# Kernel tuning notes

Hardware: AMD Instinct MI355X
Metric: run time of the kernel (lower is better)

Reference implementation:

```python
import jax, jax.numpy as jnp
import numpy as np

EPSILON = 1e-8
TAU = 0.1

def setup_inputs() -> dict:
    key = jax.random.key(0)
    x = jax.random.normal(key, (8192, 256), dtype=jnp.float32)
    return {"x": x}

def reference(x):
    # L2-normalize rows (torch F.normalize: x / max(||x||, 1e-12))
    norm = jnp.maximum(jnp.linalg.norm(x, axis=1, keepdims=True), 1e-12)
    xn = x / norm
    n = xn.shape[0]
    # pairwise cosine similarity via GEMM (equivalent to broadcast sum in source)
    cos = (xn @ xn.T) / TAU                      # [N, N]
    exp_cos = jnp.exp(cos)
    # zero out diagonal (self-similarity)
    exp_cos = exp_cos * (1.0 - jnp.eye(n, dtype=exp_cos.dtype))
    loss = jnp.log(exp_cos.sum(axis=1) / (n - 1) + EPSILON)
    return jnp.mean(loss)
```

## Files before the change

kernel.cpp:

```cpp
#include <hip/hip_runtime.h>
#include <hip/hip_bf16.h>
#include <math.h>

#define TAU_INV_LOG2E 14.4269504088896340736f
#define EPS 1e-8f

typedef __attribute__((ext_vector_type(8))) short bf16x8;
typedef __attribute__((ext_vector_type(4))) float f32x4;

static __device__ __forceinline__ unsigned short f2bf(float f) {
    unsigned int u = __float_as_uint(f);
    unsigned int r = (u + 0x7fffu + ((u >> 16) & 1u)) >> 16;
    return (unsigned short)r;
}

static __device__ __forceinline__ void glds16(const void* g, void* l) {
    __builtin_amdgcn_global_load_lds(
        (const __attribute__((address_space(1))) unsigned int*)g,
        (__attribute__((address_space(3))) unsigned int*)l,
        16, 0, 0);
}

__global__ __launch_bounds__(256) void normalize_kernel(
    const float* __restrict__ x, unsigned short* __restrict__ xn,
    float* __restrict__ out, int N) {
    const int wave = threadIdx.x >> 6;
    const int lane = threadIdx.x & 63;
    const int row  = blockIdx.x * 4 + wave;
    if (row >= N) return;

    if (blockIdx.x == 0 && threadIdx.x == 0) out[0] = 0.0f;

    const float4 v = ((const float4*)(x + (size_t)row * 256))[lane];
    float s = v.x * v.x + v.y * v.y + v.z * v.z + v.w * v.w;
    s += __shfl_xor(s, 1);
    s += __shfl_xor(s, 2);
    s += __shfl_xor(s, 4);
    s += __shfl_xor(s, 8);
    s += __shfl_xor(s, 16);
    s += __shfl_xor(s, 32);
    const float norm = fmaxf(sqrtf(s), 1e-12f);
    const float rinv = 1.0f / norm;

    ushort4 o;
    o.x = f2bf(v.x * rinv);
    o.y = f2bf(v.y * rinv);
    o.z = f2bf(v.z * rinv);
    o.w = f2bf(v.w * rinv);
    ((ushort4*)(xn + (size_t)row * 256))[lane] = o;
}

__global__ __launch_bounds__(256, 3) void gemm_exp_rowsum_kernel(
    const unsigned short* __restrict__ xn, float* __restrict__ prow, int N) {
    const int D = 256;
    __shared__ unsigned short As[2][128 * 32];
    __shared__ unsigned short Bs[2][128 * 32];

    const int tid   = threadIdx.x;
    const int wave  = tid >> 6;
    const int lane  = tid & 63;
    const int waveM = wave >> 1;
    const int waveN = wave & 1;
    const int quad  = lane >> 4;
    const int l16   = lane & 15;

    const int B = N >> 7;
    const int t = blockIdx.x;
    int bi = (int)((2.0 * B + 1.0 -
                    sqrt((2.0 * B + 1.0) * (2.0 * B + 1.0) - 8.0 * (double)t)) * 0.5);
    while (bi > 0 && t < bi * B - (bi * (bi - 1)) / 2) --bi;
    while (t >= (bi + 1) * B - ((bi + 1) * bi) / 2) ++bi;
    const int bj = bi + (t - (bi * B - (bi * (bi - 1)) / 2));
    const bool diag = (bi == bj);

    const int iBase = bi * 128;
    const int jBase = bj * 128;

    f32x4 acc[4][4];
    #pragma unroll
    for (int mt = 0; mt < 4; ++mt)
        #pragma unroll
        for (int nt = 0; nt < 4; ++nt)
            acc[mt][nt] = (f32x4){0.f, 0.f, 0.f, 0.f};

    const int lrow4 = lane >> 2;
    const int csrc  = (lane & 3) ^ ((lane >> 3) & 3);

    auto stage = [&](int buf, int k0) {
        #pragma unroll
        for (int it = 0; it < 2; ++it) {
            const int w = wave * 2 + it;
            const int r = w * 16 + lrow4;
            glds16(xn + (size_t)(iBase + r) * D + k0 + csrc * 8,
                   &As[buf][w * 512]);
            if (!diag)
                glds16(xn + (size_t)(jBase + r) * D + k0 + csrc * 8,
                       &Bs[buf][w * 512]);
        }
    };

    const int swz  = (quad ^ ((l16 >> 1) & 3)) * 8;
    const int offA = (waveM * 64 + l16) * 32 + swz;
    const int offB = (waveN * 64 + l16) * 32 + swz;
    const unsigned short* Bbase = diag ? &As[0][0] : &Bs[0][0];

    stage(0, 0);
    __syncthreads();

    #pragma unroll
    for (int kt = 0; kt < 8; ++kt) {
        const int cb = kt & 1;
        if (kt < 7) stage(cb ^ 1, (kt + 1) * 32);

        const unsigned short* Ap = &As[cb][0];
        const unsigned short* Bp = Bbase + cb * (128 * 32);
        bf16x8 a[4], b[4];
        #pragma unroll
        for (int tt = 0; tt < 4; ++tt) {
            a[tt] = *(const bf16x8*)(Ap + offA + tt * 512);
            b[tt] = *(const bf16x8*)(Bp + offB + tt * 512);
        }
        #pragma unroll
        for (int mt = 0; mt < 4; ++mt)
            #pragma unroll
            for (int nt = 0; nt < 4; ++nt)
                acc[mt][nt] = __builtin_amdgcn_mfma_f32_16x16x32_bf16(
                    a[mt], b[nt], acc[mt][nt], 0, 0, 0);

        if (kt < 7) __syncthreads();
    }

    float rsum[4][4];
    float csum[4] = {0.f, 0.f, 0.f, 0.f};
    #pragma unroll
    for (int mt = 0; mt < 4; ++mt)
        #pragma unroll
        for (int r = 0; r < 4; ++r) rsum[mt][r] = 0.f;

    #pragma unroll
    for (int mt = 0; mt < 4; ++mt) {
        const int gi0 = iBase + waveM * 64 + mt * 16 + quad * 4;
        #pragma unroll
        for (int nt = 0; nt < 4; ++nt) {
            const int gj = jBase + waveN * 64 + nt * 16 + l16;
            #pragma unroll
            for (int r = 0; r < 4; ++r) {
                float e = __builtin_amdgcn_exp2f(acc[mt][nt][r] * TAU_INV_LOG2E);
                if (gi0 + r == gj) e = 0.0f;
                rsum[mt][r] += e;
                csum[nt] += e;
            }
        }
    }
    {
        float* slot = prow + (size_t)(2 * bj + waveN) * N;
        #pragma unroll
        for (int mt = 0; mt < 4; ++mt) {
            const int gi0 = iBase + waveM * 64 + mt * 16 + quad * 4;
            #pragma unroll
            for (int r = 0; r < 4; ++r) {
                float s = rsum[mt][r];
                s += __shfl_xor(s, 1);
                s += __shfl_xor(s, 2);
                s += __shfl_xor(s, 4);
                s += __shfl_xor(s, 8);
                if (l16 == 0) slot[gi0 + r] = s;
            }
        }
    }
    if (!diag) {
        float* slot = prow + (size_t)(2 * bi + waveM) * N;
        #pragma unroll
        for (int nt = 0; nt < 4; ++nt) {
            float s = csum[nt];
            s += __shfl_xor(s, 16);
            s += __shfl_xor(s, 32);
            if (quad == 0)
                slot[jBase + waveN * 64 + nt * 16 + l16] = s;
        }
    }
}

__global__ __launch_bounds__(256) void finalize_kernel(
    const float* __restrict__ prow, float* __restrict__ out, int N) {
    __shared__ float red[4];
    const int i = blockIdx.x * 256 + threadIdx.x;
    const float inv = 1.0f / (float)(N - 1);
    float s = 0.f;
    #pragma unroll 16
    for (int p = 0; p < 128; ++p) s += prow[(size_t)p * N + i];
    float acc = logf(fmaf(s, inv, EPS));
    acc += __shfl_xor(acc, 1);
    acc += __shfl_xor(acc, 2);
    acc += __shfl_xor(acc, 4);
    acc += __shfl_xor(acc, 8);
    acc += __shfl_xor(acc, 16);
    acc += __shfl_xor(acc, 32);
    const int wave = threadIdx.x >> 6;
    const int lane = threadIdx.x & 63;
    if (lane == 0) red[wave] = acc;
    __syncthreads();
    if (threadIdx.x == 0) {
        float total = red[0] + red[1] + red[2] + red[3];
        atomicAdd(out, total / (float)N);
    }
}

extern "C" void kernel_launch(void* const* d_in, const int* in_sizes, int n_in,
                              void* d_out, int out_size, void* d_ws, size_t ws_size,
                              hipStream_t stream) {
    const float* x = (const float*)d_in[0];
    const int D = 256;
    const int N = in_sizes[0] / D;

    unsigned short* xn = (unsigned short*)d_ws;
    float* prow = (float*)((char*)d_ws + (size_t)N * D * sizeof(unsigned short));
    float* out = (float*)d_out;

    normalize_kernel<<<(N + 3) / 4, 256, 0, stream>>>(x, xn, out, N);

    const int B = N / 128;
    const int T = B * (B + 1) / 2;
    gemm_exp_rowsum_kernel<<<T, 256, 0, stream>>>(xn, prow, N);

    finalize_kernel<<<N / 256, 256, 0, stream>>>(prow, out, N);
}
```

Baseline: 95.84 us.

## Process strips of four column tiles per block with A fragments held in registers

Each block now owns one row tile and walks up to four upper-triangle column tiles. The A operand fragments stay in registers across all of them, and B fragments are read straight from global memory, so the LDS staging and barriers are gone. Row partial sums are accumulated across the strip, which cuts the number of partial-sum slots, and the finalize kernel is reworked to read variable counts of row and column partials. The cost is higher register pressure (occupancy hint drops to 2), fewer blocks, and uncoalesced 16-byte global B loads with no LDS reuse between waves.

```diff
diff --git a/kernel.cpp b/kernel.cpp
--- a/kernel.cpp
+++ b/kernel.cpp
@@ -12,13 +12,6 @@
     unsigned int u = __float_as_uint(f);
     unsigned int r = (u + 0x7fffu + ((u >> 16) & 1u)) >> 16;
     return (unsigned short)r;
-}
-
-static __device__ __forceinline__ void glds16(const void* g, void* l) {
-    __builtin_amdgcn_global_load_lds(
-        (const __attribute__((address_space(1))) unsigned int*)g,
-        (__attribute__((address_space(3))) unsigned int*)l,
-        16, 0, 0);
 }
 
 __global__ __launch_bounds__(256) void normalize_kernel(
@@ -50,12 +43,10 @@
     ((ushort4*)(xn + (size_t)row * 256))[lane] = o;
 }
 
-__global__ __launch_bounds__(256, 3) void gemm_exp_rowsum_kernel(
-    const unsigned short* __restrict__ xn, float* __restrict__ prow, int N) {
+__global__ __launch_bounds__(256, 2) void gemm_strip_kernel(
+    const unsigned short* __restrict__ xn, float* __restrict__ prowR,
+    float* __restrict__ prowC, float* __restrict__ out, int N) {
     const int D = 256;
-    __shared__ unsigned short As[2][128 * 32];
-    __shared__ unsigned short Bs[2][128 * 32];
-
     const int tid   = threadIdx.x;
     const int wave  = tid >> 6;
     const int lane  = tid & 63;
@@ -65,95 +56,87 @@
     const int l16   = lane & 15;
 
     const int B = N >> 7;
-    const int t = blockIdx.x;
-    int bi = (int)((2.0 * B + 1.0 -
-                    sqrt((2.0 * B + 1.0) * (2.0 * B + 1.0) - 8.0 * (double)t)) * 0.5);
-    while (bi > 0 && t < bi * B - (bi * (bi - 1)) / 2) --bi;
-    while (t >= (bi + 1) * B - ((bi + 1) * bi) / 2) ++bi;
-    const int bj = bi + (t - (bi * B - (bi * (bi - 1)) / 2));
-    const bool diag = (bi == bj);
-
+    int rem = blockIdx.x, bi = 0;
+    while (rem >= ((B - bi + 3) >> 2)) { rem -= (B - bi + 3) >> 2; ++bi; }
+    const int sid   = rem;
+    const int bj0   = bi + (sid << 2);
+    const int bjEnd = min(bj0 + 3, B - 1);
     const int iBase = bi * 128;
-    const int jBase = bj * 128;
-
-    f32x4 acc[4][4];
+
+    bf16x8 afr[8][4];
+    {
+        const unsigned short* aBase =
+            xn + (size_t)(iBase + waveM * 64 + l16) * D + quad * 8;
+        #pragma unroll
+        for (int kc = 0; kc < 8; ++kc)
+            #pragma unroll
+            for (int tt = 0; tt < 4; ++tt)
+                afr[kc][tt] = *(const bf16x8*)(aBase + (size_t)tt * 16 * D + kc * 32);
+    }
+
+    float rsum[4][4];
     #pragma unroll
     for (int mt = 0; mt < 4; ++mt)
         #pragma unroll
-        for (int nt = 0; nt < 4; ++nt)
-            acc[mt][nt] = (f32x4){0.f, 0.f, 0.f, 0.f};
-
-    const int lrow4 = lane >> 2;
-    const int csrc  = (lane & 3) ^ ((lane >> 3) & 3);
-
-    auto stage = [&](int buf, int k0) {
-        #pragma unroll
-        for (int it = 0; it < 2; ++it) {
-            const int w = wave * 2 + it;
-            const int r = w * 16 + lrow4;
-            glds16(xn + (size_t)(iBase + r) * D + k0 + csrc * 8,
-                   &As[buf][w * 512]);
-            if (!diag)
-                glds16(xn + (size_t)(jBase + r) * D + k0 + csrc * 8,
-                       &Bs[buf][w * 512]);
-        }
-    };
-
-    const int swz  = (quad ^ ((l16 >> 1) & 3)) * 8;
-    const int offA = (waveM * 64 + l16) * 32 + swz;
-    const int offB = (waveN * 64 + l16) * 32 + swz;
-    const unsigned short* Bbase = diag ? &As[0][0] : &Bs[0][0];
-
-    stage(0, 0);
-    __syncthreads();
-
-    #pragma unroll
-    for (int kt = 0; kt < 8; ++kt) {
-        const int cb = kt & 1;
-        if (kt < 7) stage(cb ^ 1, (kt + 1) * 32);
-
-        const unsigned short* Ap = &As[cb][0];
-        const unsigned short* Bp = Bbase + cb * (128 * 32);
-        bf16x8 a[4], b[4];
-        #pragma unroll
-        for (int tt = 0; tt < 4; ++tt) {
-            a[tt] = *(const bf16x8*)(Ap + offA + tt * 512);
-            b[tt] = *(const bf16x8*)(Bp + offB + tt * 512);
-        }
+        for (int r = 0; r < 4; ++r) rsum[mt][r] = 0.f;
+
+    for (int bj = bj0; bj <= bjEnd; ++bj) {
+        const int jBase = bj * 128;
+        const unsigned short* bBase =
+            xn + (size_t)(jBase + waveN * 64 + l16) * D + quad * 8;
+
+        f32x4 acc[4][4];
         #pragma unroll
         for (int mt = 0; mt < 4; ++mt)
             #pragma unroll
             for (int nt = 0; nt < 4; ++nt)
-                acc[mt][nt] = __builtin_amdgcn_mfma_f32_16x16x32_bf16(
-                    a[mt], b[nt], acc[mt][nt], 0, 0, 0);
-
-        if (kt < 7) __syncthreads();
+                acc[mt][nt] = (f32x4){0.f, 0.f, 0.f, 0.f};
+
+        #pragma unroll
+        for (int kc = 0; kc < 8; ++kc) {
+            bf16x8 b[4];
+            #pragma unroll
+            for (int nt = 0; nt < 4; ++nt)
+                b[nt] = *(const bf16x8*)(bBase + (size_t)nt * 16 * D + kc * 32);
+            #pragma unroll
+            for (int mt = 0; mt < 4; ++mt)
+                #pragma unroll
+                for (int nt = 0; nt < 4; ++nt)
+                    acc[mt][nt] = __builtin_amdgcn_mfma_f32_16x16x32_bf16(
+                        afr[kc][mt], b[nt], acc[mt][nt], 0, 0, 0);
+        }
+
+        float csum[4] = {0.f, 0.f, 0.f, 0.f};
+        #pragma unroll
+        for (int mt = 0; mt < 4; ++mt) {
+            const int gi0 = iBase + waveM * 64 + mt * 16 + quad * 4;
+            #pragma unroll
+            for (int nt = 0; nt < 4; ++nt) {
+                const int gj = jBase + waveN * 64 + nt * 16 + l16;
+                #pragma unroll
+                for (int r = 0; r < 4; ++r) {
+                    float e = __builtin_amdgcn_exp2f(acc[mt][nt][r] * TAU_INV_LOG2E);
+                    if (gi0 + r == gj) e = 0.0f;
+                    rsum[mt][r] += e;
+                    csum[nt] += e;
+                }
+            }
+        }
+        if (bj != bi) {
+            float* slot = prowC + (size_t)(2 * bi + waveM) * N;
+            #pragma unroll
+            for (int nt = 0; nt < 4; ++nt) {
+                float s = csum[nt];
+                s += __shfl_xor(s, 16);
+                s += __shfl_xor(s, 32);
+                if (quad == 0)
+                    slot[jBase + waveN * 64 + nt * 16 + l16] = s;
+            }
+        }
     }
 
-    float rsum[4][4];
-    float csum[4] = {0.f, 0.f, 0.f, 0.f};
-    #pragma unroll
-    for (int mt = 0; mt < 4; ++mt)
-        #pragma unroll
-        for (int r = 0; r < 4; ++r) rsum[mt][r] = 0.f;
-
-    #pragma unroll
-    for (int mt = 0; mt < 4; ++mt) {
-        const int gi0 = iBase + waveM * 64 + mt * 16 + quad * 4;
-        #pragma unroll
-        for (int nt = 0; nt < 4; ++nt) {
-            const int gj = jBase + waveN * 64 + nt * 16 + l16;
-            #pragma unroll
-            for (int r = 0; r < 4; ++r) {
-                float e = __builtin_amdgcn_exp2f(acc[mt][nt][r] * TAU_INV_LOG2E);
-                if (gi0 + r == gj) e = 0.0f;
-                rsum[mt][r] += e;
-                csum[nt] += e;
-            }
-        }
-    }
     {
-        float* slot = prow + (size_t)(2 * bj + waveN) * N;
+        float* slot = prowR + (size_t)(2 * sid + waveN) * N;
         #pragma unroll
         for (int mt = 0; mt < 4; ++mt) {
             const int gi0 = iBase + waveM * 64 + mt * 16 + quad * 4;
@@ -168,28 +151,21 @@
             }
         }
     }
-    if (!diag) {
-        float* slot = prow + (size_t)(2 * bi + waveM) * N;
-        #pragma unroll
-        for (int nt = 0; nt < 4; ++nt) {
-            float s = csum[nt];
-            s += __shfl_xor(s, 16);
-            s += __shfl_xor(s, 32);
-            if (quad == 0)
-                slot[jBase + waveN * 64 + nt * 16 + l16] = s;
-        }
-    }
-}
-
-__global__ __launch_bounds__(256) void finalize_kernel(
-    const float* __restrict__ prow, float* __restrict__ out, int N) {
-    __shared__ float red[4];
-    const int i = blockIdx.x * 256 + threadIdx.x;
-    const float inv = 1.0f / (float)(N - 1);
+}
+
+__global__ __launch_bounds__(128) void finalize_kernel(
+    const float* __restrict__ prowR, const float* __restrict__ prowC,
+    float* __restrict__ out, int N) {
+    __shared__ float red[2];
+    const int B = N >> 7;
+    const int a = blockIdx.x;
+    const int i = a * 128 + threadIdx.x;
+    const int nR = 2 * ((B - a + 3) >> 2);
+    const int nC = 2 * a;
     float s = 0.f;
-    #pragma unroll 16
-    for (int p = 0; p < 128; ++p) s += prow[(size_t)p * N + i];
-    float acc = logf(fmaf(s, inv, EPS));
+    for (int p = 0; p < nR; ++p) s += prowR[(size_t)p * N + i];
+    for (int p = 0; p < nC; ++p) s += prowC[(size_t)p * N + i];
+    float acc = logf(fmaf(s, 1.0f / (float)(N - 1), EPS));
     acc += __shfl_xor(acc, 1);
     acc += __shfl_xor(acc, 2);
     acc += __shfl_xor(acc, 4);
@@ -200,10 +176,7 @@
     const int lane = threadIdx.x & 63;
     if (lane == 0) red[wave] = acc;
     __syncthreads();
-    if (threadIdx.x == 0) {
-        float total = red[0] + red[1] + red[2] + red[3];
-        atomicAdd(out, total / (float)N);
-    }
+    if (threadIdx.x == 0) atomicAdd(out, (red[0] + red[1]) / (float)N);
 }
 
 extern "C" void kernel_launch(void* const* d_in, const int* in_sizes, int n_in,
@@ -212,16 +185,18 @@
     const float* x = (const float*)d_in[0];
     const int D = 256;
     const int N = in_sizes[0] / D;
+    const int B = N / 128;
 
     unsigned short* xn = (unsigned short*)d_ws;
-    float* prow = (float*)((char*)d_ws + (size_t)N * D * sizeof(unsigned short));
+    float* prowR = (float*)((char*)d_ws + (size_t)N * D * 2);
+    float* prowC = prowR + (size_t)32 * N;
     float* out = (float*)d_out;
 
     normalize_kernel<<<(N + 3) / 4, 256, 0, stream>>>(x, xn, out, N);
 
-    const int B = N / 128;
-    const int T = B * (B + 1) / 2;
-    gemm_exp_rowsum_kernel<<<T, 256, 0, stream>>>(xn, prow, N);
-
-    finalize_kernel<<<N / 256, 256, 0, stream>>>(prow, out, N);
-}
+    int T = 0;
+    for (int bi = 0; bi < B; ++bi) T += (B - bi + 3) >> 2;
+    gemm_strip_kernel<<<T, 256, 0, stream>>>(xn, prowR, prowC, out, N);
+
+    finalize_kernel<<<B, 128, 0, stream>>>(prowR, prowC, out, N);
+}
```

Measured after the change: 153.2 us. +59.8%, slower.

## Enlarge GEMM tiles to 256x256 with 512 threads and split partial-sum buffers

Applied to the files above, without the earlier changes.

Moves the symmetric GEMM+exp+rowsum kernel from 128x128 tiles with 4 waves to 256x256 tiles with 8 waves, each wave now computing 128x64. K steps grow to 64, and MFMA issue is wrapped in setprio. This raises arithmetic intensity and cuts the number of tile blocks and LDS loads per FLOP. In exchange it uses 128KB of LDS per block, limiting occupancy, and it drops the diagonal-block B-load shortcut. Row and column partials now go to separate buffers, and finalize reads only the slots that were written.

```diff
diff --git a/kernel.cpp b/kernel.cpp
--- a/kernel.cpp
+++ b/kernel.cpp
@@ -50,21 +50,22 @@
     ((ushort4*)(xn + (size_t)row * 256))[lane] = o;
 }
 
-__global__ __launch_bounds__(256, 3) void gemm_exp_rowsum_kernel(
-    const unsigned short* __restrict__ xn, float* __restrict__ prow, int N) {
+__global__ __launch_bounds__(512, 2) void gemm_exp_rowsum_kernel(
+    const unsigned short* __restrict__ xn, float* __restrict__ prowR,
+    float* __restrict__ prowC, int N) {
     const int D = 256;
-    __shared__ unsigned short As[2][128 * 32];
-    __shared__ unsigned short Bs[2][128 * 32];
+    __shared__ unsigned short As[2][256 * 64];
+    __shared__ unsigned short Bs[2][256 * 64];
 
     const int tid   = threadIdx.x;
     const int wave  = tid >> 6;
     const int lane  = tid & 63;
-    const int waveM = wave >> 1;
-    const int waveN = wave & 1;
+    const int waveM = wave >> 2;
+    const int waveN = wave & 3;
     const int quad  = lane >> 4;
     const int l16   = lane & 15;
 
-    const int B = N >> 7;
+    const int B = N >> 8;
     const int t = blockIdx.x;
     int bi = (int)((2.0 * B + 1.0 -
                     sqrt((2.0 * B + 1.0) * (2.0 * B + 1.0) - 8.0 * (double)t)) * 0.5);
@@ -73,73 +74,80 @@
     const int bj = bi + (t - (bi * B - (bi * (bi - 1)) / 2));
     const bool diag = (bi == bj);
 
-    const int iBase = bi * 128;
-    const int jBase = bj * 128;
-
-    f32x4 acc[4][4];
-    #pragma unroll
-    for (int mt = 0; mt < 4; ++mt)
+    const int iBase = bi * 256;
+    const int jBase = bj * 256;
+
+    f32x4 acc[8][4];
+    #pragma unroll
+    for (int mt = 0; mt < 8; ++mt)
         #pragma unroll
         for (int nt = 0; nt < 4; ++nt)
             acc[mt][nt] = (f32x4){0.f, 0.f, 0.f, 0.f};
 
-    const int lrow4 = lane >> 2;
-    const int csrc  = (lane & 3) ^ ((lane >> 3) & 3);
+    const int lrow8 = lane >> 3;
+    const int csrc  = (lane & 7) ^ ((lane >> 3) & 7);
 
     auto stage = [&](int buf, int k0) {
         #pragma unroll
-        for (int it = 0; it < 2; ++it) {
-            const int w = wave * 2 + it;
-            const int r = w * 16 + lrow4;
+        for (int it = 0; it < 4; ++it) {
+            const int r = wave * 32 + it * 8 + lrow8;
             glds16(xn + (size_t)(iBase + r) * D + k0 + csrc * 8,
-                   &As[buf][w * 512]);
-            if (!diag)
-                glds16(xn + (size_t)(jBase + r) * D + k0 + csrc * 8,
-                       &Bs[buf][w * 512]);
+                   &As[buf][(wave * 32 + it * 8) * 64]);
+            glds16(xn + (size_t)(jBase + r) * D + k0 + csrc * 8,
+                   &Bs[buf][(wave * 32 + it * 8) * 64]);
         }
     };
 
-    const int swz  = (quad ^ ((l16 >> 1) & 3)) * 8;
-    const int offA = (waveM * 64 + l16) * 32 + swz;
-    const int offB = (waveN * 64 + l16) * 32 + swz;
-    const unsigned short* Bbase = diag ? &As[0][0] : &Bs[0][0];
+    const int swz0 = ((0 * 4 + quad) ^ (l16 & 7)) * 8;
+    const int swz1 = ((1 * 4 + quad) ^ (l16 & 7)) * 8;
+    const int rowA = waveM * 128 + l16;
+    const int rowB = waveN * 64 + l16;
 
     stage(0, 0);
     __syncthreads();
 
     #pragma unroll
-    for (int kt = 0; kt < 8; ++kt) {
+    for (int kt = 0; kt < 4; ++kt) {
         const int cb = kt & 1;
-        if (kt < 7) stage(cb ^ 1, (kt + 1) * 32);
+        if (kt < 3) stage(cb ^ 1, (kt + 1) * 64);
 
         const unsigned short* Ap = &As[cb][0];
-        const unsigned short* Bp = Bbase + cb * (128 * 32);
-        bf16x8 a[4], b[4];
-        #pragma unroll
-        for (int tt = 0; tt < 4; ++tt) {
-            a[tt] = *(const bf16x8*)(Ap + offA + tt * 512);
-            b[tt] = *(const bf16x8*)(Bp + offB + tt * 512);
-        }
-        #pragma unroll
-        for (int mt = 0; mt < 4; ++mt)
+        const unsigned short* Bp = &Bs[cb][0];
+
+        #pragma unroll
+        for (int ks = 0; ks < 2; ++ks) {
+            const int swz = ks ? swz1 : swz0;
+            bf16x8 a[8], b[4];
+            #pragma unroll
+            for (int mt = 0; mt < 8; ++mt)
+                a[mt] = *(const bf16x8*)(Ap + (rowA + mt * 16) * 64 + swz);
             #pragma unroll
             for (int nt = 0; nt < 4; ++nt)
-                acc[mt][nt] = __builtin_amdgcn_mfma_f32_16x16x32_bf16(
-                    a[mt], b[nt], acc[mt][nt], 0, 0, 0);
-
-        if (kt < 7) __syncthreads();
-    }
-
-    float rsum[4][4];
+                b[nt] = *(const bf16x8*)(Bp + (rowB + nt * 16) * 64 + swz);
+
+            __builtin_amdgcn_s_setprio(1);
+            #pragma unroll
+            for (int mt = 0; mt < 8; ++mt)
+                #pragma unroll
+                for (int nt = 0; nt < 4; ++nt)
+                    acc[mt][nt] = __builtin_amdgcn_mfma_f32_16x16x32_bf16(
+                        a[mt], b[nt], acc[mt][nt], 0, 0, 0);
+            __builtin_amdgcn_s_setprio(0);
+        }
+
+        if (kt < 3) __syncthreads();
+    }
+
+    float rsum[8][4];
     float csum[4] = {0.f, 0.f, 0.f, 0.f};
     #pragma unroll
-    for (int mt = 0; mt < 4; ++mt)
+    for (int mt = 0; mt < 8; ++mt)
         #pragma unroll
         for (int r = 0; r < 4; ++r) rsum[mt][r] = 0.f;
 
     #pragma unroll
-    for (int mt = 0; mt < 4; ++mt) {
-        const int gi0 = iBase + waveM * 64 + mt * 16 + quad * 4;
+    for (int mt = 0; mt < 8; ++mt) {
+        const int gi0 = iBase + waveM * 128 + mt * 16 + quad * 4;
         #pragma unroll
         for (int nt = 0; nt < 4; ++nt) {
             const int gj = jBase + waveN * 64 + nt * 16 + l16;
@@ -153,10 +161,10 @@
         }
     }
     {
-        float* slot = prow + (size_t)(2 * bj + waveN) * N;
-        #pragma unroll
-        for (int mt = 0; mt < 4; ++mt) {
-            const int gi0 = iBase + waveM * 64 + mt * 16 + quad * 4;
+        float* slot = prowR + (size_t)(4 * bj + waveN) * N;
+        #pragma unroll
+        for (int mt = 0; mt < 8; ++mt) {
+            const int gi0 = iBase + waveM * 128 + mt * 16 + quad * 4;
             #pragma unroll
             for (int r = 0; r < 4; ++r) {
                 float s = rsum[mt][r];
@@ -169,7 +177,7 @@
         }
     }
     if (!diag) {
-        float* slot = prow + (size_t)(2 * bi + waveM) * N;
+        float* slot = prowC + (size_t)(2 * bi + waveM) * N;
         #pragma unroll
         for (int nt = 0; nt < 4; ++nt) {
             float s = csum[nt];
@@ -182,14 +190,15 @@
 }
 
 __global__ __launch_bounds__(256) void finalize_kernel(
-    const float* __restrict__ prow, float* __restrict__ out, int N) {
+    const float* __restrict__ prowR, const float* __restrict__ prowC,
+    float* __restrict__ out, int N) {
     __shared__ float red[4];
-    const int i = blockIdx.x * 256 + threadIdx.x;
-    const float inv = 1.0f / (float)(N - 1);
+    const int a = blockIdx.x;
+    const int i = a * 256 + threadIdx.x;
     float s = 0.f;
-    #pragma unroll 16
-    for (int p = 0; p < 128; ++p) s += prow[(size_t)p * N + i];
-    float acc = logf(fmaf(s, inv, EPS));
+    for (int p = 4 * a; p < 128; ++p) s += prowR[(size_t)p * N + i];
+    for (int p = 0; p < 2 * a; ++p)   s += prowC[(size_t)p * N + i];
+    float acc = logf(fmaf(s, 1.0f / (float)(N - 1), EPS));
     acc += __shfl_xor(acc, 1);
     acc += __shfl_xor(acc, 2);
     acc += __shfl_xor(acc, 4);
@@ -200,10 +209,8 @@
     const int lane = threadIdx.x & 63;
     if (lane == 0) red[wave] = acc;
     __syncthreads();
-    if (threadIdx.x == 0) {
-        float total = red[0] + red[1] + red[2] + red[3];
-        atomicAdd(out, total / (float)N);
-    }
+    if (threadIdx.x == 0)
+        atomicAdd(out, (red[0] + red[1] + red[2] + red[3]) / (float)N);
 }
 
 extern "C" void kernel_launch(void* const* d_in, const int* in_sizes, int n_in,
@@ -212,16 +219,17 @@
     const float* x = (const float*)d_in[0];
     const int D = 256;
     const int N = in_sizes[0] / D;
+    const int B = N / 256;
 
     unsigned short* xn = (unsigned short*)d_ws;
-    float* prow = (float*)((char*)d_ws + (size_t)N * D * sizeof(unsigned short));
+    float* prowR = (float*)((char*)d_ws + (size_t)N * D * 2);
+    float* prowC = prowR + (size_t)128 * N;
     float* out = (float*)d_out;
 
     normalize_kernel<<<(N + 3) / 4, 256, 0, stream>>>(x, xn, out, N);
 
-    const int B = N / 128;
     const int T = B * (B + 1) / 2;
-    gemm_exp_rowsum_kernel<<<T, 256, 0, stream>>>(xn, prow, N);
-
-    finalize_kernel<<<N / 256, 256, 0, stream>>>(prow, out, N);
-}
+    gemm_exp_rowsum_kernel<<<T, 512, 0, stream>>>(xn, prowR, prowC, N);
+
+    finalize_kernel<<<B, 256, 0, stream>>>(prowR, prowC, out, N);
+}
```

Result: slower. 131.8 us (+37.5%).
